# Performance work log

Hardware: AMD Instinct MI355X
Metric: run time of the kernel (lower is better)

Reference implementation:

```python
import jax, jax.numpy as jnp
from jax import lax
import numpy as np

SCALES = [1.0, 0.9, 0.8, 0.7, 0.6]
SOFTMAX_SCALE = 10.0
RES_SCALE = 1.0
EPS = 1e-4  # escape_NaN buffer


def prelu(x, a):
    # torch nn.PReLU with a single shared parameter a
    return jnp.where(x >= 0, x, a * x)


def conv1x1(x, W, b):
    # x: [B,Cin,H,W], W: [Cout,Cin], b: [Cout]
    return jnp.einsum('oi,bihw->bohw', W, x) + b[None, :, None, None]


def extract_patches(x):
    # x: [B,C,H,W] -> [B, H*W, C, 3, 3]; 'same' padding (pad 1), stride 1,
    # matching F.unfold channel ordering (C, kh, kw) and row-major spatial order.
    B, C, H, W = x.shape
    p = jnp.pad(x, ((0, 0), (0, 0), (1, 1), (1, 1)))
    shifts = [p[:, :, i:i + H, j:j + W] for i in range(3) for j in range(3)]
    pat = jnp.stack(shifts, axis=-1)                      # [B,C,H,W,9]
    pat = pat.reshape(B, C, H, W, 3, 3)
    return pat.transpose(0, 2, 3, 1, 4, 5).reshape(B, H * W, C, 3, 3)


def setup_inputs() -> dict:
    key = jax.random.key(0)
    ks = jax.random.split(key, 7)
    B, C, H, W = 4, 64, 48, 48
    red = 2
    x = jax.random.normal(ks[0], (B, C, H, W), jnp.float32)
    # conv_match_L_base: 1x1 conv 64->32 + PReLU
    Wb = jax.random.normal(ks[1], (C // red, C), jnp.float32) * 0.05
    bb = jax.random.normal(ks[2], (C // red,), jnp.float32) * 0.05
    ab = jnp.asarray(0.25, jnp.float32)
    # conv_match: 1x1 conv 64->32 + PReLU
    Wm = jax.random.normal(ks[3], (C // red, C), jnp.float32) * 0.05
    bm = jax.random.normal(ks[4], (C // red,), jnp.float32) * 0.05
    am = jnp.asarray(0.25, jnp.float32)
    # conv_assembly: 1x1 conv 64->64 + PReLU
    Wa = jax.random.normal(ks[5], (C, C), jnp.float32) * 0.05
    ba = jax.random.normal(ks[6], (C,), jnp.float32) * 0.05
    aa = jnp.asarray(0.25, jnp.float32)
    return {"x": x, "Wb": Wb, "bb": bb, "ab": ab,
            "Wm": Wm, "bm": bm, "am": am,
            "Wa": Wa, "ba": ba, "aa": aa}


def reference(x, Wb, bb, ab, Wm, bm, am, Wa, ba, aa):
    B, C, H, W = x.shape
    match_base = prelu(conv1x1(x, Wb, bb), ab)  # [B,32,H,W]

    w_list, raw_list = [], []
    for s in SCALES:
        if s != 1.0:
            Hs, Ws = int(H * s), int(W * s)
            ref = jax.image.resize(x, (B, C, Hs, Ws), 'bilinear', antialias=False)
        else:
            ref = x
        base = prelu(conv1x1(ref, Wa, ba), aa)   # [B,64,Hs,Ws]
        mat = prelu(conv1x1(ref, Wm, bm), am)    # [B,32,Hs,Ws]
        raw_list.append(extract_patches(base))   # [B,Ls,64,3,3]
        w_list.append(extract_patches(mat))      # [B,Ls,32,3,3]

    wall = jnp.concatenate(w_list, axis=1)       # [B,N,32,3,3]
    rawall = jnp.concatenate(raw_list, axis=1)   # [B,N,64,3,3]
    norm = jnp.maximum(jnp.sqrt(jnp.sum(wall * wall, axis=(2, 3, 4), keepdims=True)), EPS)
    wn = wall / norm

    dn = ('NCHW', 'OIHW', 'NCHW')

    def per_sample(xb, wb, rb):
        # xb: [32,H,W], wb: [N,32,3,3], rb: [N,64,3,3]
        scores = lax.conv_general_dilated(xb[None], wb, (1, 1), ((1, 1), (1, 1)),
                                          dimension_numbers=dn)       # [1,N,H,W]
        attn = jax.nn.softmax(scores * SOFTMAX_SCALE, axis=1)
        # conv_transpose2d(attn, rb, stride=1, padding=1) == conv with flipped,
        # channel-swapped kernel and padding 1
        kt = jnp.flip(rb, axis=(2, 3)).transpose(1, 0, 2, 3)           # [64,N,3,3]
        out = lax.conv_general_dilated(attn, kt, (1, 1), ((1, 1), (1, 1)),
                                       dimension_numbers=dn)           # [1,64,H,W]
        return out[0] / 4.0

    y = jax.vmap(per_sample)(match_base, wn, rawall)  # [B,64,H,W]
    return y + x * RES_SCALE
```

## Files before the change

kernel.cpp:

```cpp
#include <hip/hip_runtime.h>
#include <hip/hip_bf16.h>
#include <hip/hip_fp16.h>

typedef __half h16;
typedef _Float16 f16;
typedef f16 f16x8 __attribute__((ext_vector_type(8)));
typedef __attribute__((ext_vector_type(4))) float f32x4;

#define NB 4
#define NCH 64
#define HW 2304
#define NP 7470
#define NPAD 7552
#define NT 236
#define NBLK 59
#define SW2 NPAD

__device__ __forceinline__ float us2f(unsigned short u){
  unsigned v = (unsigned)u << 16; float f; __builtin_memcpy(&f, &v, 4); return f;
}
__device__ __forceinline__ void gl16(const void* g, void* l){
  __builtin_amdgcn_global_load_lds((const __attribute__((address_space(1))) unsigned int*)g,
                                   (__attribute__((address_space(3))) unsigned int*)l, 16, 0, 0);
}

__device__ __forceinline__ void n_decode(int n, int& off, int& d, int& y, int& x){
  if (n < 2304)      { off = 0;    d = 48; }
  else if (n < 4153) { off = 2304; d = 43; }
  else if (n < 5597) { off = 4153; d = 38; }
  else if (n < 6686) { off = 5597; d = 33; }
  else               { off = 6686; d = 28; }
  int l = n - off; y = l / d; x = l - y * d;
}

__global__ __launch_bounds__(256) void k_detect(const void* __restrict__ x, int* __restrict__ flag){
  const unsigned short* u = (const unsigned short*)x;
  int tid = threadIdx.x;
  int c = 0;
  for (int i = tid; i < 8192; i += 256){
    float v = us2f(u[i]);
    float a = fabsf(v);
    if (v == 0.f || (a > 1e-5f && a < 1e3f)) c++;
  }
  #pragma unroll
  for (int o = 1; o < 64; o <<= 1) c += __shfl_xor(c, o);
  __shared__ int wr[4];
  if ((tid & 63) == 0) wr[tid >> 6] = c;
  __syncthreads();
  if (tid == 0) flag[0] = ((wr[0]+wr[1]+wr[2]+wr[3]) > 7000) ? 1 : 0;
}

struct CanonArgs { const void* src[10]; float* dst[10]; int end[10]; };

__global__ __launch_bounds__(256) void k_canon_all(CanonArgs a, int tot, const int* __restrict__ flag){
  int id = blockIdx.x * 256 + threadIdx.x;
  if (id >= tot) return;
  int k = 0;
  while (id >= a.end[k]) k++;
  int local = id - (k ? a.end[k-1] : 0);
  float v;
  if (flag[0]) v = us2f(((const unsigned short*)a.src[k])[local]);
  else         v = ((const float*)a.src[k])[local];
  a.dst[k][local] = v;
}

__global__ __launch_bounds__(256) void k_resize(const float* __restrict__ x, h16* __restrict__ xs){
  int id = blockIdx.x * 256 + threadIdx.x;
  if (id >= NB * NCH * NP) return;
  int b = id / (NCH*NP), rem = id - b*(NCH*NP);
  int c = rem / NP, n = rem - c*NP;
  int off, d, y, xx; n_decode(n, off, d, y, xx);
  const float* pc = x + ((size_t)b * NCH + c) * HW;
  float v;
  if (off == 0){
    v = pc[y*48 + xx];
  } else {
    float cy = (y + 0.5f) * (48.0f / (float)d) - 0.5f;
    float cx = (xx + 0.5f) * (48.0f / (float)d) - 0.5f;
    int y0 = (int)floorf(cy), x0 = (int)floorf(cx);
    float fy = cy - (float)y0, fx = cx - (float)x0;
    int y1 = min(y0 + 1, 47), x1 = min(x0 + 1, 47);
    y0 = max(y0, 0); x0 = max(x0, 0);
    v = (1.f-fy)*((1.f-fx)*pc[y0*48+x0] + fx*pc[y0*48+x1])
      + fy*((1.f-fx)*pc[y1*48+x0] + fx*pc[y1*48+x1]);
  }
  xs[id] = __float2half(v);
}

template<bool OB>
__global__ __launch_bounds__(256) void k_conv1x1(const h16* __restrict__ in, const float* __restrict__ Wt,
    const float* __restrict__ bias, const float* __restrict__ alpha, void* __restrict__ outv,
    int npix, int cout, size_t in_bstride, size_t out_bstride, int rs_in, int rs_out){
  __shared__ float Wl[64*64];
  __shared__ float it[64][64];
  int b = blockIdx.y;
  int n0 = blockIdx.x * 64;
  int tid = threadIdx.x;
  const h16* ib = in + (size_t)b * in_bstride;
  for (int i = tid; i < cout * 64; i += 256) Wl[i] = Wt[i];
  for (int i = tid; i < 64 * 64; i += 256){
    int ci = i >> 6, nn = i & 63;
    int n = n0 + nn;
    it[ci][nn] = (n < npix) ? __half2float(ib[(size_t)ci * rs_in + n]) : 0.f;
  }
  __syncthreads();
  float al = alpha[0];
  for (int oi = tid; oi < cout * 64; oi += 256){
    int co = oi >> 6, nn = oi & 63;
    float acc = bias[co];
    #pragma unroll
    for (int ci = 0; ci < 64; ci++) acc = fmaf(Wl[co*64+ci], it[ci][nn], acc);
    acc = acc >= 0.f ? acc : al * acc;
    int n = n0 + nn;
    if (n < npix){
      size_t idx = (size_t)b * out_bstride + (size_t)co * rs_out + n;
      if constexpr (OB) ((h16*)outv)[idx] = __float2half(acc);
      else              ((float*)outv)[idx] = acc;
    }
  }
}

__global__ __launch_bounds__(256) void k_sq(const float* __restrict__ mat, float* __restrict__ q){
  int id = blockIdx.x * 256 + threadIdx.x;
  if (id >= NB * NP) return;
  int b = id / NP, n = id - b * NP;
  const float* mp = mat + (size_t)b * 32 * NP + n;
  float s = 0.f;
  #pragma unroll
  for (int c = 0; c < 32; c++){ float v = mp[(size_t)c * NP]; s += v * v; }
  q[id] = s;
}

__global__ __launch_bounds__(256) void k_ninv(const float* __restrict__ q, float* __restrict__ ninv){
  int id = blockIdx.x * 256 + threadIdx.x;
  if (id >= NB * NP) return;
  int b = id / NP, n = id - b * NP;
  int off, d, y, x; n_decode(n, off, d, y, x);
  const float* qb = q + (size_t)b * NP + off;
  float s = 0.f;
  #pragma unroll
  for (int dy = -1; dy <= 1; dy++){
    int yy = y + dy; if (yy < 0 || yy >= d) continue;
    #pragma unroll
    for (int dx = -1; dx <= 1; dx++){
      int xx = x + dx; if (xx < 0 || xx >= d) continue;
      s += qb[yy * d + xx];
    }
  }
  ninv[id] = 1.f / fmaxf(sqrtf(s), 1e-4f);
}

__global__ __launch_bounds__(256) void k_packU(const float* __restrict__ mb, h16* __restrict__ U){
  int id = blockIdx.x * 256 + threadIdx.x;
  if (id >= NB * HW * 288) return;
  int b = id / (HW*288), rem = id - b*(HW*288);
  int p = rem / 288, k = rem - p * 288;
  int c = k / 9, r = k - c * 9, kh = r / 3, kw = r - kh * 3;
  int y = p / 48 + kh - 1, x = (p % 48) + kw - 1;
  float v = 0.f;
  if (y >= 0 && y < 48 && x >= 0 && x < 48)
    v = mb[((size_t)b * 32 + c) * HW + y * 48 + x];
  U[id] = __float2half(v);
}

__global__ __launch_bounds__(256) void k_packW(const float* __restrict__ mat, const float* __restrict__ ninv,
                                               h16* __restrict__ Wp, int b0, int g){
  int id = blockIdx.x * 256 + threadIdx.x;
  if (id >= g * NPAD * 288) return;
  int bg = id / (NPAD*288), rem = id - bg*(NPAD*288);
  int n = rem / 288, k = rem - n * 288;
  float v = 0.f;
  if (n < NP){
    int b = b0 + bg;
    int c = k / 9, r = k - c * 9, kh = r / 3, kw = r - kh * 3;
    int off, d, y, x; n_decode(n, off, d, y, x);
    int yy = y + kh - 1, xx = x + kw - 1;
    if (yy >= 0 && yy < d && xx >= 0 && xx < d)
      v = mat[((size_t)b * 32 + c) * NP + off + yy * d + xx] * 10.f * ninv[(size_t)b*NP + n];
  }
  Wp[id] = __float2half(v);
}

__global__ __launch_bounds__(256) void k_packR(const h16* __restrict__ src, h16* __restrict__ dst){
  int id = blockIdx.x * 256 + threadIdx.x;
  if (id >= NB * NT * 576 * 32) return;
  int b = id / (NT*576*32), rem = id - b*(NT*576*32);
  int t = rem / (576*32), rem2 = rem - t*(576*32);
  int j = rem2 / 32, kl = rem2 - j*32;
  int n = t*32 + kl;
  h16 v = __float2half(0.f);
  if (n < NP){
    int c = j / 9, r = j - c * 9, kh = r / 3, kw = r - kh * 3;
    int off, d, y, x; n_decode(n, off, d, y, x);
    int yy = y + kh - 1, xx = x + kw - 1;
    if (yy >= 0 && yy < d && xx >= 0 && xx < d)
      v = src[((size_t)b * 64 + c) * NP + off + yy * d + xx];
  }
  dst[id] = v;
}

__global__ __launch_bounds__(512) void k_gemm1m(const f16* __restrict__ U, const f16* __restrict__ Wp,
    h16* __restrict__ S16, float* __restrict__ Pm, float* __restrict__ Ps, int b0){
  int bg = blockIdx.z, b = b0 + bg;
  int m0 = blockIdx.y * 128, n0 = blockIdx.x * 128;
  int tid = threadIdx.x, l = tid & 63, w = tid >> 6;
  int wm = w >> 1, wn = w & 1;
  int ch = l >> 4, cl = l & 15;
  __shared__ __align__(16) char At[3][8192];
  __shared__ __align__(16) char Bt[3][8192];
  __shared__ float mred[128][2];
  __shared__ float sred[128][2];
  f32x4 acc[2][4] = {};
  const f16* Ub = U + ((size_t)b * HW + m0) * 288;
  const f16* Wb = Wp + ((size_t)bg * NPAD + n0) * 288;
  int abyte[2], bbyte[4];
  #pragma unroll
  for (int mt = 0; mt < 2; mt++){
    int lr = wm*32 + mt*16 + cl;
    abyte[mt] = lr*64 + ((ch ^ ((lr>>1)&3))<<4);
  }
  #pragma unroll
  for (int nt = 0; nt < 4; nt++){
    int lr = wn*64 + nt*16 + cl;
    bbyte[nt] = lr*64 + ((ch ^ ((lr>>1)&3))<<4);
  }
  int srow = tid >> 2, scs = (tid & 3) ^ ((srow >> 1) & 3);
  auto STAGE1 = [&](int t, int bi){
    gl16(Ub + (size_t)srow*288 + t*32 + scs*8, At[bi] + tid*16);
    gl16(Wb + (size_t)srow*288 + t*32 + scs*8, Bt[bi] + tid*16);
  };
  STAGE1(0, 0);
  STAGE1(1, 1);
  __syncthreads();
  int cur = 0;
  for (int t = 0; t < 9; ++t){
    int nx = cur + 2; if (nx >= 3) nx -= 3;
    if (t + 2 < 9){
      STAGE1(t + 2, nx);
      asm volatile("s_waitcnt vmcnt(4)" ::: "memory");
    } else if (t + 1 < 9){
      asm volatile("s_waitcnt vmcnt(2)" ::: "memory");
    } else {
      asm volatile("s_waitcnt vmcnt(0)" ::: "memory");
    }
    __builtin_amdgcn_s_barrier();
    asm volatile("" ::: "memory");
    f16x8 a[2], bv[4];
    #pragma unroll
    for (int mt = 0; mt < 2; mt++) a[mt] = *reinterpret_cast<const f16x8*>(At[cur] + abyte[mt]);
    #pragma unroll
    for (int nt = 0; nt < 4; nt++) bv[nt] = *reinterpret_cast<const f16x8*>(Bt[cur] + bbyte[nt]);
    #pragma unroll
    for (int mt = 0; mt < 2; mt++)
      #pragma unroll
      for (int nt = 0; nt < 4; nt++)
        acc[mt][nt] = __builtin_amdgcn_mfma_f32_16x16x32_f16(a[mt], bv[nt], acc[mt][nt], 0, 0, 0);
    asm volatile("s_waitcnt lgkmcnt(0)" ::: "memory");
    __builtin_amdgcn_s_barrier();
    cur = cur + 1; if (cur >= 3) cur -= 3;
  }
  #pragma unroll
  for (int mt = 0; mt < 2; mt++)
    #pragma unroll
    for (int i = 0; i < 4; i++){
      float v = -3e38f;
      #pragma unroll
      for (int nt = 0; nt < 4; nt++){
        int gn = n0 + wn*64 + nt*16 + cl;
        float t = acc[mt][nt][i];
        v = fmaxf(v, (gn < NP) ? t : -3e38f);
      }
      v = fmaxf(v, __shfl_xor(v, 1));
      v = fmaxf(v, __shfl_xor(v, 2));
      v = fmaxf(v, __shfl_xor(v, 4));
      v = fmaxf(v, __shfl_xor(v, 8));
      if (cl == 0) mred[wm*32 + mt*16 + ch*4 + i][wn] = v;
    }
  __syncthreads();
  #pragma unroll
  for (int mt = 0; mt < 2; mt++)
    #pragma unroll
    for (int i = 0; i < 4; i++){
      int r = wm*32 + mt*16 + ch*4 + i;
      float Ml = fmaxf(mred[r][0], mred[r][1]);
      int gm = m0 + r;
      float s = 0.f;
      #pragma unroll
      for (int nt = 0; nt < 4; nt++){
        int gn = n0 + wn*64 + nt*16 + cl;
        float e = (gn < NP) ? __expf(acc[mt][nt][i] - Ml) : 0.f;
        S16[((size_t)bg*HW + gm)*SW2 + gn] = __float2half(e);
        s += e;
      }
      s += __shfl_xor(s, 1);
      s += __shfl_xor(s, 2);
      s += __shfl_xor(s, 4);
      s += __shfl_xor(s, 8);
      if (cl == 0) sred[r][wn] = s;
    }
  __syncthreads();
  if (tid < 128){
    float Mf = fmaxf(mred[tid][0], mred[tid][1]);
    float L  = sred[tid][0] + sred[tid][1];
    size_t o = ((size_t)bg*HW + m0 + tid)*NBLK + blockIdx.x;
    Pm[o] = Mf; Ps[o] = L;
  }
}

__global__ __launch_bounds__(256) void k_sfac(const float* __restrict__ Pm, const float* __restrict__ Ps,
                                              float* __restrict__ Fac, int gc){
  int rid = blockIdx.x * 4 + (threadIdx.x >> 6);
  int lane = threadIdx.x & 63;
  if (rid >= gc * HW) return;
  const float* pm = Pm + (size_t)rid * NBLK;
  const float* ps = Ps + (size_t)rid * NBLK;
  float mv = (lane < NBLK) ? pm[lane] : -3e38f;
  float sv = (lane < NBLK) ? ps[lane] : 0.f;
  float M = mv;
  #pragma unroll
  for (int o = 1; o < 64; o <<= 1) M = fmaxf(M, __shfl_xor(M, o));
  float e = (lane < NBLK) ? __expf(mv - M) : 0.f;
  float c = e * sv;
  #pragma unroll
  for (int o = 1; o < 64; o <<= 1) c += __shfl_xor(c, o);
  float inv = 1.f / c;
  if (lane < NBLK) Fac[(size_t)rid * NBLK + lane] = e * inv;
}

__global__ __launch_bounds__(512) void k_gemm2n(const f16* __restrict__ S16, const f16* __restrict__ RpT,
    const float* __restrict__ Fac, h16* __restrict__ T, int b0){
  int nwg = gridDim.x;
  int p = blockIdx.x;
  int L = (nwg % 8 == 0) ? ((p & 7)*(nwg>>3) + (p>>3)) : p;
  int jh = L % 3; int t1 = L / 3; int my = t1 % 18; int bg = t1 / 18;
  int b = b0 + bg;
  int m0 = my * 128;
  int tid = threadIdx.x, l = tid & 63, w = tid >> 6;
  int wm = w >> 2, wc = w & 3;
  int ch = l >> 4, cl = l & 15;
  __shared__ __align__(16) char smem[56320];
  f32x4 acc[4][3] = {};
  int lrm[4], abyte[4], rbyte[3];
  #pragma unroll
  for (int mt = 0; mt < 4; mt++){
    lrm[mt] = wm*64 + mt*16 + cl;
    abyte[mt] = lrm[mt]*64 + ((ch ^ ((lrm[mt]>>1)&3))<<4);
  }
  #pragma unroll
  for (int nt = 0; nt < 3; nt++){
    int jr = wc*48 + nt*16 + cl;
    rbyte[nt] = jr*64 + ((ch ^ ((jr>>1)&3))<<4);
  }
  const f16* Sb  = S16 + ((size_t)bg*HW + m0)*SW2;
  const f16* Rb0 = RpT + (size_t)b*((size_t)NT*576*32) + (size_t)jh*(192*32);
  const float* facb = Fac + ((size_t)bg*HW + m0)*NBLK;

  auto STAGE = [&](int t, int bi){
    char* dS = smem + bi*8192;
    char* dR = smem + 16384 + bi*12288;
    const f16* Rb = Rb0 + (size_t)t*(576*32);
    {
      int row = tid >> 2, cs = (tid & 3) ^ ((row >> 1) & 3);
      gl16(Sb + (size_t)row*SW2 + t*32 + cs*8, dS + tid*16);
    }
    {
      int row = tid >> 2, cs = (tid & 3) ^ ((row >> 1) & 3);
      gl16(Rb + (size_t)row*32 + cs*8, dR + tid*16);
    }
    if (tid < 256){
      int i2 = tid + 512;
      int r2 = i2 >> 2, c2 = (i2 & 3) ^ ((r2 >> 1) & 3);
      gl16(Rb + (size_t)r2*32 + c2*8, dR + i2*16);
    }
  };

  {
    f16* fl = (f16*)(smem + 40960);
    for (int i = tid; i < NBLK*128; i += 512){
      int nb = i >> 7, mm = i & 127;
      fl[i] = (f16)facb[(size_t)mm*NBLK + nb];
    }
  }
  STAGE(0, 0);
  __syncthreads();

  int cur = 0;
  for (int t = 0; t < NT; ++t){
    if (t + 1 < NT){
      STAGE(t + 1, cur ^ 1);
      if (tid < 256) { asm volatile("s_waitcnt vmcnt(3)" ::: "memory"); }
      else           { asm volatile("s_waitcnt vmcnt(2)" ::: "memory"); }
    } else {
      asm volatile("s_waitcnt vmcnt(0)" ::: "memory");
    }
    __builtin_amdgcn_s_barrier();
    asm volatile("" ::: "memory");
    const char* Sc = smem + cur*8192;
    const char* Rc = smem + 16384 + cur*12288;
    const f16* fl = (const f16*)(smem + 40960);
    int nb = t >> 2;
    f16x8 pa[4];
    #pragma unroll
    for (int mt = 0; mt < 4; mt++){
      f16 fac = fl[nb*128 + lrm[mt]];
      f16x8 sv = *reinterpret_cast<const f16x8*>(Sc + abyte[mt]);
      pa[mt] = sv * fac;
    }
    #pragma unroll
    for (int nt = 0; nt < 3; nt++){
      f16x8 bv = *reinterpret_cast<const f16x8*>(Rc + rbyte[nt]);
      #pragma unroll
      for (int mt = 0; mt < 4; mt++)
        acc[mt][nt] = __builtin_amdgcn_mfma_f32_16x16x32_f16(pa[mt], bv, acc[mt][nt], 0, 0, 0);
    }
    asm volatile("s_waitcnt lgkmcnt(0)" ::: "memory");
    __builtin_amdgcn_s_barrier();
    cur ^= 1;
  }

  {
    h16* Tl = (h16*)smem;
    #pragma unroll
    for (int nt = 0; nt < 3; nt++)
      #pragma unroll
      for (int mt = 0; mt < 4; mt++)
        #pragma unroll
        for (int i = 0; i < 4; i++)
          Tl[(wc*48 + nt*16 + cl)*136 + wm*64 + mt*16 + ch*4 + i] = __float2half(acc[mt][nt][i]);
    __syncthreads();
    #pragma unroll
    for (int rep = 0; rep < 6; rep++){
      int idx = tid + rep*512;
      int j0 = idx >> 4, q = idx & 15;
      uint4 v = *reinterpret_cast<const uint4*>((const char*)Tl + j0*272 + q*16);
      h16* dst = T + ((size_t)b*576 + jh*192 + j0)*HW + m0 + q*8;
      *reinterpret_cast<uint4*>(dst) = v;
    }
  }
}

__global__ __launch_bounds__(256) void k_fold(const h16* __restrict__ T, const float* __restrict__ x,
    void* __restrict__ out, const int* __restrict__ flag){
  int id = blockIdx.x * 256 + threadIdx.x;
  if (id >= NB * 64 * HW) return;
  int b = id / (64*HW), id2 = id - b*(64*HW);
  int co = id2 / HW, p = id2 - co * HW;
  int y = p / 48, xx = p - y * 48;
  float acc = 0.f;
  #pragma unroll
  for (int dy = -1; dy <= 1; dy++){
    int yy = y + dy; if (yy < 0 || yy >= 48) continue;
    #pragma unroll
    for (int dx = -1; dx <= 1; dx++){
      int x2 = xx + dx; if (x2 < 0 || x2 >= 48) continue;
      int j = co*9 + (1-dy)*3 + (1-dx);
      acc += __half2float(T[((size_t)b*576 + j)*HW + yy*48 + x2]);
    }
  }
  size_t gi = (size_t)id;
  float r = x[gi] + 0.25f * acc;
  if (flag[0]) ((__hip_bfloat16*)out)[gi] = __float2bfloat16(r);
  else         ((float*)out)[gi] = r;
}

extern "C" void kernel_launch(void* const* d_in, const int* in_sizes, int n_in,
                              void* d_out, int out_size, void* d_ws, size_t ws_size,
                              hipStream_t stream){
  (void)out_size; (void)n_in;

  char* cur = (char*)d_ws;
  auto carve = [&](size_t bytes)->char*{
    char* p = cur; cur += (bytes + 255) & ~(size_t)255; return p;
  };
  int*   flag  = (int*)  carve(4);
  float* canon[10];
  for (int i = 0; i < 10; i++) canon[i] = (float*)carve((size_t)in_sizes[i] * 4);
  float* xc = canon[0];
  float* Wb = canon[1]; float* bb = canon[2]; float* ab = canon[3];
  float* Wm = canon[4]; float* bm = canon[5]; float* am = canon[6];
  float* Wa = canon[7]; float* ba = canon[8]; float* aa = canon[9];

  h16*   xs    = (h16*)  carve((size_t)NB * 64 * NP * 2);
  float* mbuf  = (float*)carve((size_t)NB * 32 * HW * 4);
  float* mat   = (float*)carve((size_t)NB * 32 * NP * 4);
  float* qbuf  = (float*)carve((size_t)NB * NP * 4);
  float* ninv  = (float*)carve((size_t)NB * NP * 4);
  h16*   baseh = (h16*)  carve((size_t)NB * 64 * NP * 2);
  h16*   U     = (h16*)  carve((size_t)NB * HW * 288 * 2);
  h16*   RpT   = (h16*)  carve((size_t)NB * NT * 576 * 32 * 2);
  h16*   T     = (h16*)  carve((size_t)NB * 576 * HW * 2);

  size_t fixed = (size_t)(cur - (char*)d_ws);
  size_t perb  = (((size_t)NPAD*288*2 + 255) & ~(size_t)255)
               + (((size_t)HW*SW2*2 + 255) & ~(size_t)255)
               + 3 * (((size_t)HW*NBLK*4 + 255) & ~(size_t)255);
  size_t avail = (ws_size > fixed) ? ws_size - fixed : 0;
  int g = (int)(avail / perb);
  if (g < 1) g = 1;
  if (g > NB) g = NB;
  h16*   Wp  = (h16*)  carve((size_t)g * NPAD * 288 * 2);
  h16*   S16 = (h16*)  carve((size_t)g * HW * SW2 * 2);
  float* Pm  = (float*)carve((size_t)g * HW * NBLK * 4);
  float* Ps  = (float*)carve((size_t)g * HW * NBLK * 4);
  float* Fac = (float*)carve((size_t)g * HW * NBLK * 4);

  k_detect<<<1, 256, 0, stream>>>(d_in[0], flag);
  {
    CanonArgs ca; int tot = 0;
    for (int i = 0; i < 10; i++){
      ca.src[i] = d_in[i]; ca.dst[i] = canon[i];
      tot += in_sizes[i]; ca.end[i] = tot;
    }
    k_canon_all<<<(tot + 255)/256, 256, 0, stream>>>(ca, tot, flag);
  }

  k_resize<<<((size_t)NB*NCH*NP + 255)/256, 256, 0, stream>>>(xc, xs);

  dim3 gm((NP + 63)/64, NB);
  k_conv1x1<false><<<gm, 256, 0, stream>>>(xs, Wm, bm, am, (void*)mat,   NP, 32, (size_t)64*NP, (size_t)32*NP, NP, NP);
  k_conv1x1<true ><<<gm, 256, 0, stream>>>(xs, Wa, ba, aa, (void*)baseh, NP, 64, (size_t)64*NP, (size_t)64*NP, NP, NP);
  dim3 gb2((HW + 63)/64, NB);
  k_conv1x1<false><<<gb2, 256, 0, stream>>>(xs, Wb, bb, ab, (void*)mbuf, HW, 32, (size_t)64*NP, (size_t)32*HW, NP, HW);

  k_sq  <<<(NB*NP + 255)/256, 256, 0, stream>>>(mat, qbuf);
  k_ninv<<<(NB*NP + 255)/256, 256, 0, stream>>>(qbuf, ninv);
  k_packU<<<((size_t)NB*HW*288 + 255)/256, 256, 0, stream>>>(mbuf, U);
  k_packR<<<((size_t)NB*NT*576*32 + 255)/256, 256, 0, stream>>>(baseh, RpT);

  for (int b0 = 0; b0 < NB; b0 += g){
    int gc = (b0 + g <= NB) ? g : (NB - b0);
    k_packW<<<((size_t)gc*NPAD*288 + 255)/256, 256, 0, stream>>>(mat, ninv, Wp, b0, gc);
    dim3 g1(NBLK, HW/128, gc);
    k_gemm1m<<<g1, 512, 0, stream>>>((const f16*)U, (const f16*)Wp, S16, Pm, Ps, b0);
    k_sfac<<<(gc*HW + 3)/4, 256, 0, stream>>>(Pm, Ps, Fac, gc);
    int nwg2 = 3 * 18 * gc;
    k_gemm2n<<<nwg2, 512, 0, stream>>>((const f16*)S16, (const f16*)RpT, Fac, T, b0);
  }

  k_fold<<<(NB*64*HW + 255)/256, 256, 0, stream>>>(T, xc, d_out, flag);
}
```

Measured before the change: 366.7 us.

## Split-K the second GEMM into two halves and widen per-wave tiles in both GEMMs

Both GEMM kernels drop from 512 to 256 threads per block, so each wave computes a larger output tile: 64x64 in the first GEMM and 64x96 in the second. The second GEMM also splits its K range (the N patches) into two halves launched as separate workgroups, which doubles the grid. Each half writes a partial result into its own T buffer, and the fold kernel adds the two. The aim is to raise occupancy and grid fill for the long-K second GEMM and to get more MFMA reuse per LDS load, at the cost of twice the T memory, extra partial-sum traffic, and higher register pressure.

```diff
diff --git a/kernel.cpp b/kernel.cpp
--- a/kernel.cpp
+++ b/kernel.cpp
@@ -13,6 +13,7 @@
 #define NP 7470
 #define NPAD 7552
 #define NT 236
+#define NT2 118
 #define NBLK 59
 #define SW2 NPAD
 
@@ -199,7 +200,7 @@
   dst[id] = v;
 }
 
-__global__ __launch_bounds__(512) void k_gemm1m(const f16* __restrict__ U, const f16* __restrict__ Wp,
+__global__ __launch_bounds__(256) void k_gemm1m(const f16* __restrict__ U, const f16* __restrict__ Wp,
     h16* __restrict__ S16, float* __restrict__ Pm, float* __restrict__ Ps, int b0){
   int bg = blockIdx.z, b = b0 + bg;
   int m0 = blockIdx.y * 128, n0 = blockIdx.x * 128;
@@ -210,13 +211,13 @@
   __shared__ __align__(16) char Bt[3][8192];
   __shared__ float mred[128][2];
   __shared__ float sred[128][2];
-  f32x4 acc[2][4] = {};
+  f32x4 acc[4][4] = {};
   const f16* Ub = U + ((size_t)b * HW + m0) * 288;
   const f16* Wb = Wp + ((size_t)bg * NPAD + n0) * 288;
-  int abyte[2], bbyte[4];
-  #pragma unroll
-  for (int mt = 0; mt < 2; mt++){
-    int lr = wm*32 + mt*16 + cl;
+  int abyte[4], bbyte[4];
+  #pragma unroll
+  for (int mt = 0; mt < 4; mt++){
+    int lr = wm*64 + mt*16 + cl;
     abyte[mt] = lr*64 + ((ch ^ ((lr>>1)&3))<<4);
   }
   #pragma unroll
@@ -224,34 +225,38 @@
     int lr = wn*64 + nt*16 + cl;
     bbyte[nt] = lr*64 + ((ch ^ ((lr>>1)&3))<<4);
   }
-  int srow = tid >> 2, scs = (tid & 3) ^ ((srow >> 1) & 3);
-  auto STAGE1 = [&](int t, int bi){
-    gl16(Ub + (size_t)srow*288 + t*32 + scs*8, At[bi] + tid*16);
-    gl16(Wb + (size_t)srow*288 + t*32 + scs*8, Bt[bi] + tid*16);
+  auto ST1 = [&](int t, int bi){
+    #pragma unroll
+    for (int rep = 0; rep < 2; rep++){
+      int i = tid + rep*256;
+      int row = i >> 2, cs = (i & 3) ^ ((row >> 1) & 3);
+      gl16(Ub + (size_t)row*288 + t*32 + cs*8, At[bi] + i*16);
+      gl16(Wb + (size_t)row*288 + t*32 + cs*8, Bt[bi] + i*16);
+    }
   };
-  STAGE1(0, 0);
-  STAGE1(1, 1);
+  ST1(0, 0);
+  ST1(1, 1);
   __syncthreads();
   int cur = 0;
   for (int t = 0; t < 9; ++t){
     int nx = cur + 2; if (nx >= 3) nx -= 3;
     if (t + 2 < 9){
-      STAGE1(t + 2, nx);
+      ST1(t + 2, nx);
+      asm volatile("s_waitcnt vmcnt(8)" ::: "memory");
+    } else if (t + 1 < 9){
       asm volatile("s_waitcnt vmcnt(4)" ::: "memory");
-    } else if (t + 1 < 9){
-      asm volatile("s_waitcnt vmcnt(2)" ::: "memory");
     } else {
       asm volatile("s_waitcnt vmcnt(0)" ::: "memory");
     }
     __builtin_amdgcn_s_barrier();
     asm volatile("" ::: "memory");
-    f16x8 a[2], bv[4];
-    #pragma unroll
-    for (int mt = 0; mt < 2; mt++) a[mt] = *reinterpret_cast<const f16x8*>(At[cur] + abyte[mt]);
+    f16x8 a[4], bv[4];
+    #pragma unroll
+    for (int mt = 0; mt < 4; mt++) a[mt] = *reinterpret_cast<const f16x8*>(At[cur] + abyte[mt]);
     #pragma unroll
     for (int nt = 0; nt < 4; nt++) bv[nt] = *reinterpret_cast<const f16x8*>(Bt[cur] + bbyte[nt]);
     #pragma unroll
-    for (int mt = 0; mt < 2; mt++)
+    for (int mt = 0; mt < 4; mt++)
       #pragma unroll
       for (int nt = 0; nt < 4; nt++)
         acc[mt][nt] = __builtin_amdgcn_mfma_f32_16x16x32_f16(a[mt], bv[nt], acc[mt][nt], 0, 0, 0);
@@ -260,7 +265,7 @@
     cur = cur + 1; if (cur >= 3) cur -= 3;
   }
   #pragma unroll
-  for (int mt = 0; mt < 2; mt++)
+  for (int mt = 0; mt < 4; mt++)
     #pragma unroll
     for (int i = 0; i < 4; i++){
       float v = -3e38f;
@@ -274,14 +279,14 @@
       v = fmaxf(v, __shfl_xor(v, 2));
       v = fmaxf(v, __shfl_xor(v, 4));
       v = fmaxf(v, __shfl_xor(v, 8));
-      if (cl == 0) mred[wm*32 + mt*16 + ch*4 + i][wn] = v;
+      if (cl == 0) mred[wm*64 + mt*16 + ch*4 + i][wn] = v;
     }
   __syncthreads();
   #pragma unroll
-  for (int mt = 0; mt < 2; mt++)
+  for (int mt = 0; mt < 4; mt++)
     #pragma unroll
     for (int i = 0; i < 4; i++){
-      int r = wm*32 + mt*16 + ch*4 + i;
+      int r = wm*64 + mt*16 + ch*4 + i;
       float Ml = fmaxf(mred[r][0], mred[r][1]);
       int gm = m0 + r;
       float s = 0.f;
@@ -327,69 +332,71 @@
   if (lane < NBLK) Fac[(size_t)rid * NBLK + lane] = e * inv;
 }
 
-__global__ __launch_bounds__(512) void k_gemm2n(const f16* __restrict__ S16, const f16* __restrict__ RpT,
+__global__ __launch_bounds__(256) void k_gemm2n(const f16* __restrict__ S16, const f16* __restrict__ RpT,
     const float* __restrict__ Fac, h16* __restrict__ T, int b0){
   int nwg = gridDim.x;
   int p = blockIdx.x;
   int L = (nwg % 8 == 0) ? ((p & 7)*(nwg>>3) + (p>>3)) : p;
-  int jh = L % 3; int t1 = L / 3; int my = t1 % 18; int bg = t1 / 18;
+  int jh = L % 3; int t1 = L / 3; int my = t1 % 18; int t2 = t1 / 18;
+  int ks = t2 & 1;  int bg = t2 >> 1;
   int b = b0 + bg;
   int m0 = my * 128;
   int tid = threadIdx.x, l = tid & 63, w = tid >> 6;
-  int wm = w >> 2, wc = w & 3;
+  int wm = w >> 1, wc = w & 1;
   int ch = l >> 4, cl = l & 15;
-  __shared__ __align__(16) char smem[56320];
-  f32x4 acc[4][3] = {};
-  int lrm[4], abyte[4], rbyte[3];
+  __shared__ __align__(16) char smem[48640];
+  f32x4 acc[4][6] = {};
+  int lrm[4], abyte[4], rbyte[6];
   #pragma unroll
   for (int mt = 0; mt < 4; mt++){
     lrm[mt] = wm*64 + mt*16 + cl;
     abyte[mt] = lrm[mt]*64 + ((ch ^ ((lrm[mt]>>1)&3))<<4);
   }
   #pragma unroll
-  for (int nt = 0; nt < 3; nt++){
-    int jr = wc*48 + nt*16 + cl;
+  for (int nt = 0; nt < 6; nt++){
+    int jr = wc*96 + nt*16 + cl;
     rbyte[nt] = jr*64 + ((ch ^ ((jr>>1)&3))<<4);
   }
   const f16* Sb  = S16 + ((size_t)bg*HW + m0)*SW2;
   const f16* Rb0 = RpT + (size_t)b*((size_t)NT*576*32) + (size_t)jh*(192*32);
   const float* facb = Fac + ((size_t)bg*HW + m0)*NBLK;
+  int nb0 = (ks*NT2) >> 2;
 
   auto STAGE = [&](int t, int bi){
     char* dS = smem + bi*8192;
     char* dR = smem + 16384 + bi*12288;
     const f16* Rb = Rb0 + (size_t)t*(576*32);
-    {
-      int row = tid >> 2, cs = (tid & 3) ^ ((row >> 1) & 3);
-      gl16(Sb + (size_t)row*SW2 + t*32 + cs*8, dS + tid*16);
-    }
-    {
-      int row = tid >> 2, cs = (tid & 3) ^ ((row >> 1) & 3);
-      gl16(Rb + (size_t)row*32 + cs*8, dR + tid*16);
-    }
-    if (tid < 256){
-      int i2 = tid + 512;
-      int r2 = i2 >> 2, c2 = (i2 & 3) ^ ((r2 >> 1) & 3);
-      gl16(Rb + (size_t)r2*32 + c2*8, dR + i2*16);
+    #pragma unroll
+    for (int rep = 0; rep < 2; rep++){
+      int i = tid + rep*256;
+      int row = i >> 2, cs = (i & 3) ^ ((row >> 1) & 3);
+      gl16(Sb + (size_t)row*SW2 + t*32 + cs*8, dS + i*16);
+    }
+    #pragma unroll
+    for (int rep = 0; rep < 3; rep++){
+      int i = tid + rep*256;
+      int row = i >> 2, cs = (i & 3) ^ ((row >> 1) & 3);
+      gl16(Rb + (size_t)row*32 + cs*8, dR + i*16);
     }
   };
 
   {
     f16* fl = (f16*)(smem + 40960);
-    for (int i = tid; i < NBLK*128; i += 512){
-      int nb = i >> 7, mm = i & 127;
-      fl[i] = (f16)facb[(size_t)mm*NBLK + nb];
-    }
-  }
-  STAGE(0, 0);
+    for (int i = tid; i < 30*128; i += 256){
+      int nbl = i >> 7, mm = i & 127;
+      int nb = nb0 + nbl;
+      fl[i] = (nb < NBLK) ? (f16)facb[(size_t)mm*NBLK + nb] : (f16)0.f;
+    }
+  }
+  STAGE(ks*NT2, 0);
   __syncthreads();
 
   int cur = 0;
-  for (int t = 0; t < NT; ++t){
-    if (t + 1 < NT){
+  for (int tt = 0; tt < NT2; ++tt){
+    int t = ks*NT2 + tt;
+    if (tt + 1 < NT2){
       STAGE(t + 1, cur ^ 1);
-      if (tid < 256) { asm volatile("s_waitcnt vmcnt(3)" ::: "memory"); }
-      else           { asm volatile("s_waitcnt vmcnt(2)" ::: "memory"); }
+      asm volatile("s_waitcnt vmcnt(5)" ::: "memory");
     } else {
       asm volatile("s_waitcnt vmcnt(0)" ::: "memory");
     }
@@ -398,16 +405,16 @@
     const char* Sc = smem + cur*8192;
     const char* Rc = smem + 16384 + cur*12288;
     const f16* fl = (const f16*)(smem + 40960);
-    int nb = t >> 2;
+    int nbl = (t >> 2) - nb0;
     f16x8 pa[4];
     #pragma unroll
     for (int mt = 0; mt < 4; mt++){
-      f16 fac = fl[nb*128 + lrm[mt]];
+      f16 fac = fl[nbl*128 + lrm[mt]];
       f16x8 sv = *reinterpret_cast<const f16x8*>(Sc + abyte[mt]);
       pa[mt] = sv * fac;
     }
     #pragma unroll
-    for (int nt = 0; nt < 3; nt++){
+    for (int nt = 0; nt < 6; nt++){
       f16x8 bv = *reinterpret_cast<const f16x8*>(Rc + rbyte[nt]);
       #pragma unroll
       for (int mt = 0; mt < 4; mt++)
@@ -418,22 +425,27 @@
     cur ^= 1;
   }
 
-  {
-    h16* Tl = (h16*)smem;
-    #pragma unroll
-    for (int nt = 0; nt < 3; nt++)
+  h16* Tsp = T + (size_t)ks * ((size_t)NB*576*HW);
+  h16* Tl = (h16*)smem;
+  #pragma unroll
+  for (int r = 0; r < 2; ++r){
+    __syncthreads();
+    if (wc == r){
       #pragma unroll
-      for (int mt = 0; mt < 4; mt++)
+      for (int nt = 0; nt < 6; nt++)
         #pragma unroll
-        for (int i = 0; i < 4; i++)
-          Tl[(wc*48 + nt*16 + cl)*136 + wm*64 + mt*16 + ch*4 + i] = __float2half(acc[mt][nt][i]);
+        for (int mt = 0; mt < 4; mt++)
+          #pragma unroll
+          for (int i = 0; i < 4; i++)
+            Tl[(nt*16 + cl)*136 + wm*64 + mt*16 + ch*4 + i] = __float2half(acc[mt][nt][i]);
+    }
     __syncthreads();
     #pragma unroll
     for (int rep = 0; rep < 6; rep++){
-      int idx = tid + rep*512;
+      int idx = tid + rep*256;
       int j0 = idx >> 4, q = idx & 15;
       uint4 v = *reinterpret_cast<const uint4*>((const char*)Tl + j0*272 + q*16);
-      h16* dst = T + ((size_t)b*576 + jh*192 + j0)*HW + m0 + q*8;
+      h16* dst = Tsp + ((size_t)b*576 + jh*192 + r*96 + j0)*HW + m0 + q*8;
       *reinterpret_cast<uint4*>(dst) = v;
     }
   }
@@ -441,6 +453,7 @@
 
 __global__ __launch_bounds__(256) void k_fold(const h16* __restrict__ T, const float* __restrict__ x,
     void* __restrict__ out, const int* __restrict__ flag){
+  const h16* T2 = T + (size_t)NB*576*HW;
   int id = blockIdx.x * 256 + threadIdx.x;
   if (id >= NB * 64 * HW) return;
   int b = id / (64*HW), id2 = id - b*(64*HW);
@@ -454,7 +467,8 @@
     for (int dx = -1; dx <= 1; dx++){
       int x2 = xx + dx; if (x2 < 0 || x2 >= 48) continue;
       int j = co*9 + (1-dy)*3 + (1-dx);
-      acc += __half2float(T[((size_t)b*576 + j)*HW + yy*48 + x2]);
+      size_t o = ((size_t)b*576 + j)*HW + yy*48 + x2;
+      acc += __half2float(T[o]) + __half2float(T2[o]);
     }
   }
   size_t gi = (size_t)id;
@@ -488,7 +502,7 @@
   h16*   baseh = (h16*)  carve((size_t)NB * 64 * NP * 2);
   h16*   U     = (h16*)  carve((size_t)NB * HW * 288 * 2);
   h16*   RpT   = (h16*)  carve((size_t)NB * NT * 576 * 32 * 2);
-  h16*   T     = (h16*)  carve((size_t)NB * 576 * HW * 2);
+  h16*   T     = (h16*)  carve((size_t)2 * NB * 576 * HW * 2);
 
   size_t fixed = (size_t)(cur - (char*)d_ws);
   size_t perb  = (((size_t)NPAD*288*2 + 255) & ~(size_t)255)
@@ -531,10 +545,10 @@
     int gc = (b0 + g <= NB) ? g : (NB - b0);
     k_packW<<<((size_t)gc*NPAD*288 + 255)/256, 256, 0, stream>>>(mat, ninv, Wp, b0, gc);
     dim3 g1(NBLK, HW/128, gc);
-    k_gemm1m<<<g1, 512, 0, stream>>>((const f16*)U, (const f16*)Wp, S16, Pm, Ps, b0);
+    k_gemm1m<<<g1, 256, 0, stream>>>((const f16*)U, (const f16*)Wp, S16, Pm, Ps, b0);
     k_sfac<<<(gc*HW + 3)/4, 256, 0, stream>>>(Pm, Ps, Fac, gc);
-    int nwg2 = 3 * 18 * gc;
-    k_gemm2n<<<nwg2, 512, 0, stream>>>((const f16*)S16, (const f16*)RpT, Fac, T, b0);
+    int nwg2 = 3 * 18 * 2 * gc;
+    k_gemm2n<<<nwg2, 256, 0, stream>>>((const f16*)S16, (const f16*)RpT, Fac, T, b0);
   }
 
   k_fold<<<(NB*64*HW + 255)/256, 256, 0, stream>>>(T, xc, d_out, flag);
```

New measurement: 381.0 us. 3.9% more time.

## Split-K the second GEMM into two halves with a partial-sum buffer

Applied to the files above, without the earlier changes.

Splits the K loop of k_gemm2n into two halves handled by separate workgroups, doubling the grid so more CUs stay busy. Each half writes its fp16 partial result to its own copy of T, and k_fold adds the two copies. The epilogue staging is done in two passes to fit the smaller shared buffer, and s_setprio is raised around the MFMA section. The cost is twice the T writes and reads, plus extra fp16 rounding of the partial sums.

```diff
diff --git a/kernel.cpp b/kernel.cpp
--- a/kernel.cpp
+++ b/kernel.cpp
@@ -13,6 +13,7 @@
 #define NP 7470
 #define NPAD 7552
 #define NT 236
+#define NT2 118
 #define NBLK 59
 #define SW2 NPAD
 
@@ -332,13 +333,14 @@
   int nwg = gridDim.x;
   int p = blockIdx.x;
   int L = (nwg % 8 == 0) ? ((p & 7)*(nwg>>3) + (p>>3)) : p;
-  int jh = L % 3; int t1 = L / 3; int my = t1 % 18; int bg = t1 / 18;
+  int jh = L % 3; int t1 = L / 3; int my = t1 % 18; int t2 = t1 / 18;
+  int ks = t2 & 1;  int bg = t2 >> 1;
   int b = b0 + bg;
   int m0 = my * 128;
   int tid = threadIdx.x, l = tid & 63, w = tid >> 6;
   int wm = w >> 2, wc = w & 3;
   int ch = l >> 4, cl = l & 15;
-  __shared__ __align__(16) char smem[56320];
+  __shared__ __align__(16) char smem[48640];
   f32x4 acc[4][3] = {};
   int lrm[4], abyte[4], rbyte[3];
   #pragma unroll
@@ -354,6 +356,7 @@
   const f16* Sb  = S16 + ((size_t)bg*HW + m0)*SW2;
   const f16* Rb0 = RpT + (size_t)b*((size_t)NT*576*32) + (size_t)jh*(192*32);
   const float* facb = Fac + ((size_t)bg*HW + m0)*NBLK;
+  int nb0 = (ks*NT2) >> 2;
 
   auto STAGE = [&](int t, int bi){
     char* dS = smem + bi*8192;
@@ -362,9 +365,6 @@
     {
       int row = tid >> 2, cs = (tid & 3) ^ ((row >> 1) & 3);
       gl16(Sb + (size_t)row*SW2 + t*32 + cs*8, dS + tid*16);
-    }
-    {
-      int row = tid >> 2, cs = (tid & 3) ^ ((row >> 1) & 3);
       gl16(Rb + (size_t)row*32 + cs*8, dR + tid*16);
     }
     if (tid < 256){
@@ -376,17 +376,19 @@
 
   {
     f16* fl = (f16*)(smem + 40960);
-    for (int i = tid; i < NBLK*128; i += 512){
-      int nb = i >> 7, mm = i & 127;
-      fl[i] = (f16)facb[(size_t)mm*NBLK + nb];
-    }
-  }
-  STAGE(0, 0);
+    for (int i = tid; i < 30*128; i += 512){
+      int nbl = i >> 7, mm = i & 127;
+      int nb = nb0 + nbl;
+      fl[i] = (nb < NBLK) ? (f16)facb[(size_t)mm*NBLK + nb] : (f16)0.f;
+    }
+  }
+  STAGE(ks*NT2, 0);
   __syncthreads();
 
   int cur = 0;
-  for (int t = 0; t < NT; ++t){
-    if (t + 1 < NT){
+  for (int tt = 0; tt < NT2; ++tt){
+    int t = ks*NT2 + tt;
+    if (tt + 1 < NT2){
       STAGE(t + 1, cur ^ 1);
       if (tid < 256) { asm volatile("s_waitcnt vmcnt(3)" ::: "memory"); }
       else           { asm volatile("s_waitcnt vmcnt(2)" ::: "memory"); }
@@ -398,11 +400,12 @@
     const char* Sc = smem + cur*8192;
     const char* Rc = smem + 16384 + cur*12288;
     const f16* fl = (const f16*)(smem + 40960);
-    int nb = t >> 2;
+    int nbl = (t >> 2) - nb0;
+    __builtin_amdgcn_s_setprio(1);
     f16x8 pa[4];
     #pragma unroll
     for (int mt = 0; mt < 4; mt++){
-      f16 fac = fl[nb*128 + lrm[mt]];
+      f16 fac = fl[nbl*128 + lrm[mt]];
       f16x8 sv = *reinterpret_cast<const f16x8*>(Sc + abyte[mt]);
       pa[mt] = sv * fac;
     }
@@ -413,27 +416,33 @@
       for (int mt = 0; mt < 4; mt++)
         acc[mt][nt] = __builtin_amdgcn_mfma_f32_16x16x32_f16(pa[mt], bv, acc[mt][nt], 0, 0, 0);
     }
+    __builtin_amdgcn_s_setprio(0);
     asm volatile("s_waitcnt lgkmcnt(0)" ::: "memory");
     __builtin_amdgcn_s_barrier();
     cur ^= 1;
   }
 
-  {
-    h16* Tl = (h16*)smem;
-    #pragma unroll
-    for (int nt = 0; nt < 3; nt++)
+  h16* Tsp = T + (size_t)ks * ((size_t)NB*576*HW);
+  h16* Tl = (h16*)smem;
+  #pragma unroll
+  for (int r = 0; r < 2; ++r){
+    __syncthreads();
+    if ((wc >> 1) == r){
       #pragma unroll
-      for (int mt = 0; mt < 4; mt++)
+      for (int nt = 0; nt < 3; nt++)
         #pragma unroll
-        for (int i = 0; i < 4; i++)
-          Tl[(wc*48 + nt*16 + cl)*136 + wm*64 + mt*16 + ch*4 + i] = __float2half(acc[mt][nt][i]);
+        for (int mt = 0; mt < 4; mt++)
+          #pragma unroll
+          for (int i = 0; i < 4; i++)
+            Tl[((wc & 1)*48 + nt*16 + cl)*136 + wm*64 + mt*16 + ch*4 + i] = __float2half(acc[mt][nt][i]);
+    }
     __syncthreads();
     #pragma unroll
-    for (int rep = 0; rep < 6; rep++){
+    for (int rep = 0; rep < 3; rep++){
       int idx = tid + rep*512;
       int j0 = idx >> 4, q = idx & 15;
       uint4 v = *reinterpret_cast<const uint4*>((const char*)Tl + j0*272 + q*16);
-      h16* dst = T + ((size_t)b*576 + jh*192 + j0)*HW + m0 + q*8;
+      h16* dst = Tsp + ((size_t)b*576 + jh*192 + r*96 + j0)*HW + m0 + q*8;
       *reinterpret_cast<uint4*>(dst) = v;
     }
   }
@@ -441,6 +450,7 @@
 
 __global__ __launch_bounds__(256) void k_fold(const h16* __restrict__ T, const float* __restrict__ x,
     void* __restrict__ out, const int* __restrict__ flag){
+  const h16* T2 = T + (size_t)NB*576*HW;
   int id = blockIdx.x * 256 + threadIdx.x;
   if (id >= NB * 64 * HW) return;
   int b = id / (64*HW), id2 = id - b*(64*HW);
@@ -454,7 +464,8 @@
     for (int dx = -1; dx <= 1; dx++){
       int x2 = xx + dx; if (x2 < 0 || x2 >= 48) continue;
       int j = co*9 + (1-dy)*3 + (1-dx);
-      acc += __half2float(T[((size_t)b*576 + j)*HW + yy*48 + x2]);
+      size_t o = ((size_t)b*576 + j)*HW + yy*48 + x2;
+      acc += __half2float(T[o]) + __half2float(T2[o]);
     }
   }
   size_t gi = (size_t)id;
@@ -488,7 +499,7 @@
   h16*   baseh = (h16*)  carve((size_t)NB * 64 * NP * 2);
   h16*   U     = (h16*)  carve((size_t)NB * HW * 288 * 2);
   h16*   RpT   = (h16*)  carve((size_t)NB * NT * 576 * 32 * 2);
-  h16*   T     = (h16*)  carve((size_t)NB * 576 * HW * 2);
+  h16*   T     = (h16*)  carve((size_t)2 * NB * 576 * HW * 2);
 
   size_t fixed = (size_t)(cur - (char*)d_ws);
   size_t perb  = (((size_t)NPAD*288*2 + 255) & ~(size_t)255)
@@ -533,7 +544,7 @@
     dim3 g1(NBLK, HW/128, gc);
     k_gemm1m<<<g1, 512, 0, stream>>>((const f16*)U, (const f16*)Wp, S16, Pm, Ps, b0);
     k_sfac<<<(gc*HW + 3)/4, 256, 0, stream>>>(Pm, Ps, Fac, gc);
-    int nwg2 = 3 * 18 * gc;
+    int nwg2 = 3 * 18 * 2 * gc;
     k_gemm2n<<<nwg2, 512, 0, stream>>>((const f16*)S16, (const f16*)RpT, Fac, T, b0);
   }
 
```

Measured after the change: 343.7 us. 6.3% less time.
